# Kernel tuning notes

Hardware: AMD Instinct MI355X
Metric: run time of the kernel (lower is better)

The kernel has to match this reference:

```python
import jax, jax.numpy as jnp
from jax import lax
import numpy as np

B, C, H, Wd = 32, 128, 56, 56
FILTERS = 128
KH = KW = 3
T_MIN_PREV = 0.0  # module defaults (set_params never called)
T_MIN = 0.0
T_MAX = 1.0


def setup_inputs() -> dict:
    key = jax.random.key(0)
    k1, k2 = jax.random.split(key)
    tj = jax.random.uniform(k1, (B, C, H, Wd), dtype=jnp.float32)          # spike times
    W = jax.random.normal(k2, (C * KH * KW, FILTERS), dtype=jnp.float32) * 0.02  # kernel.view(-1, filters)
    D_i = jnp.zeros((9, FILTERS), dtype=jnp.float32)                        # intrinsic delays (only row 0 used)
    return {"tj": tj, "W": W, "D_i": D_i}


def reference(tj, W, D_i):
    # 'same' padding with value t_min, then unfold + (tj - t_min) @ W is
    # exactly a zero-padded conv on (tj - t_min): the pad entries become 0.
    x = tj - T_MIN                                   # [B,C,H,W]
    # Unfold orders patch rows as (C, kh, kw); build the equivalent OIHW kernel.
    kernel = jnp.transpose(W.reshape(C, KH, KW, FILTERS), (3, 0, 1, 2))  # [F,C,KH,KW]
    y = lax.conv_general_dilated(
        x, kernel, window_strides=(1, 1), padding="SAME",
        dimension_numbers=("NCHW", "OIHW", "NCHW"))    # [B,F,H,W]
    threshold = T_MAX - T_MIN - D_i[0]                 # [F]
    ti = y + threshold[None, :, None, None] + T_MIN
    ti = jnp.minimum(ti, T_MAX)                        # torch.where(ti < t_max, ti, t_max)
    return jnp.transpose(ti, (0, 2, 3, 1))             # [B,H,W,F], matches ti.view(b,H,W,filters)
```

## Files before the change

kernel.cpp:

```cpp
#include <hip/hip_runtime.h>


#define BZ 32
#define CC 128
#define HH 56
#define WWD 56
#define HWP 3136
#define FF 128
#define PH 58
#define PW 58
#define NSTEP 36
#define AB_BYTES 24576
#define A_GRAN_REAL 1392
#define BOFF 49152
#define BB_BYTES 8192
#define LDS_TOTAL 73728

typedef __attribute__((ext_vector_type(8))) __bf16 bf16x8;
typedef __attribute__((ext_vector_type(4))) float f32x4;
typedef __attribute__((ext_vector_type(8))) unsigned short us8;
typedef __attribute__((ext_vector_type(4))) float flt4;

__device__ __forceinline__ unsigned short f2bf(float f) {
  unsigned int u = __float_as_uint(f);
  unsigned int r = (u + 0x7FFFu + ((u >> 16) & 1u)) >> 16;
  return (unsigned short)r;
}

#define GLOAD_LDS16(g, l)                                                              \
  __builtin_amdgcn_global_load_lds((const __attribute__((address_space(1))) void*)(g), \
                                   (__attribute__((address_space(3))) void*)(l), 16, 0, 0)

__global__ void prep_w_kernel(const float* __restrict__ W, unsigned short* __restrict__ Wt) {
  int idx = blockIdx.x * 256 + threadIdx.x;
  if (idx >= NSTEP * 512) return;
  int qr = idx >> 9;
  int g = idx & 511;
  int q = qr / 9, r = qr - q * 9;
  int f = g >> 2, kg = g & 3;
  us8 v;
#pragma unroll
  for (int j = 0; j < 8; ++j) {
    int c = q * 32 + kg * 8 + j;
    v[j] = f2bf(W[(c * 9 + r) * FF + f]);
  }
  *reinterpret_cast<us8*>(Wt + (size_t)idx * 8) = v;
}

__global__ __launch_bounds__(256) void prep_x_kernel(const float* __restrict__ x,
                                                     unsigned short* __restrict__ xp) {
  const int blk = blockIdx.x;
  const int b = blk / PH;
  const int ph = blk - b * PH;
  const int tid = threadIdx.x;
  unsigned short* dst = xp + (size_t)(b * PH + ph) * PW * CC;

  if (ph == 0 || ph == PH - 1) {
    us8 z;
#pragma unroll
    for (int k = 0; k < 8; ++k) z[k] = 0;
    for (int i = tid; i < PW * CC / 8; i += 256) reinterpret_cast<us8*>(dst)[i] = z;
    return;
  }

  __shared__ float sm[CC][57];
  const int h = ph - 1;
  {
    const int c = tid >> 1;
    const int half = tid & 1;
    const float* src = x + ((size_t)(b * CC + c)) * HWP + h * WWD + half * 28;
#pragma unroll
    for (int k = 0; k < 7; ++k) {
      flt4 v = *reinterpret_cast<const flt4*>(src + k * 4);
      sm[c][half * 28 + k * 4 + 0] = v[0];
      sm[c][half * 28 + k * 4 + 1] = v[1];
      sm[c][half * 28 + k * 4 + 2] = v[2];
      sm[c][half * 28 + k * 4 + 3] = v[3];
    }
  }
  __syncthreads();
  for (int i = tid; i < PW * 16; i += 256) {
    const int ww = i >> 4;
    const int cg = i & 15;
    us8 v;
    if (ww == 0 || ww == PW - 1) {
#pragma unroll
      for (int k = 0; k < 8; ++k) v[k] = 0;
    } else {
      const int w = ww - 1;
#pragma unroll
      for (int k = 0; k < 8; ++k) v[k] = f2bf(sm[cg * 8 + k][w]);
    }
    reinterpret_cast<us8*>(dst)[i] = v;
  }
}

struct Ctx {
  const unsigned short* xp;
  const unsigned short* Wt;
  int tid;
  int srcA[6];
  int gbase[7];
  int bOffB[4];
  f32x4 acc[7][4];
};

template <int S>
__device__ __forceinline__ void step(Ctx& c, unsigned char* lds) {
  constexpr int q = S / 9, r = S - q * 9;
  constexpr int dh = r / 3 - 1, dw = r - (r / 3) * 3 - 1;
  constexpr int tapoff = (dh * PW + dw) * 4;
  constexpr bool issueA = (q < 3) && (r < 6);
  constexpr bool issueB = (S <= NSTEP - 3);
  constexpr int aS = issueA ? 1 : 0;
  constexpr int bS = issueB ? 2 : 0;
  constexpr int aP = (S == 0) ? 0 : ((((S - 1) / 9) < 3 && ((S - 1) % 9) < 6) ? 1 : 0);
  constexpr int bP = (S == 0) ? 2 : (((S - 1) <= NSTEP - 3) ? 2 : 0);
  constexpr int nOut = aS + bS + aP + bP;

  if constexpr (issueA) {
    const unsigned short* src = c.xp + c.srcA[r] + (q + 1) * 32;
    unsigned char* dst = lds + ((q + 1) & 1) * AB_BYTES + (size_t)(r * 256 + c.tid) * 16;
    GLOAD_LDS16(src, dst);
  }
  if constexpr (issueB) {
    const unsigned short* src = c.Wt + (size_t)(S + 2) * 4096 + c.tid * 8;
    unsigned char* dst = lds + BOFF + ((S + 2) % 3) * BB_BYTES + (size_t)c.tid * 16;
    GLOAD_LDS16(src, dst);
    GLOAD_LDS16(src + 2048, dst + 4096);
  }
  asm volatile("s_waitcnt vmcnt(%0)" ::"n"(nOut));
  __builtin_amdgcn_s_barrier();
  __builtin_amdgcn_sched_barrier(0);

  const unsigned char* pa = lds + (q & 1) * AB_BYTES;
  const unsigned char* pb = lds + BOFF + (S % 3) * BB_BYTES;
  bf16x8 af[7], bf[4];
#pragma unroll
  for (int i = 0; i < 7; ++i)
    af[i] = *reinterpret_cast<const bf16x8*>(pa + ((c.gbase[i] + tapoff) << 4));
#pragma unroll
  for (int j = 0; j < 4; ++j)
    bf[j] = *reinterpret_cast<const bf16x8*>(pb + c.bOffB[j]);

  __builtin_amdgcn_s_setprio(1);
#pragma unroll
  for (int i = 0; i < 7; ++i)
#pragma unroll
    for (int j = 0; j < 4; ++j)
      c.acc[i][j] = __builtin_amdgcn_mfma_f32_16x16x32_bf16(af[i], bf[j], c.acc[i][j], 0, 0, 0);
  __builtin_amdgcn_s_setprio(0);
  __builtin_amdgcn_sched_barrier(0);
  __builtin_amdgcn_s_barrier();
}

template <int S>
__device__ __forceinline__ void do_steps(Ctx& c, unsigned char* lds) {
  step<S>(c, lds);
  if constexpr (S + 1 < NSTEP) do_steps<S + 1>(c, lds);
}

__global__ __launch_bounds__(256, 2) void spiking_conv_main(
    const unsigned short* __restrict__ xp, const unsigned short* __restrict__ Wt,
    const float* __restrict__ Di, float* __restrict__ out) {
  extern __shared__ unsigned char lds[];

  const int bid = blockIdx.x;
  const int wg = (bid & 7) * 56 + (bid >> 3);
  const int b = wg / 14;
  const int rg = wg - b * 14;
  const int h0 = rg * 4;

  Ctx c;
  c.xp = xp;
  c.Wt = Wt;
  const int tid = threadIdx.x;
  c.tid = tid;
  const int lane = tid & 63, wv = tid >> 6;
  const int wr = wv >> 1, wc = wv & 1;
  const int frow = lane & 15, kg = lane >> 4;

#pragma unroll
  for (int k = 0; k < 6; ++k) {
    int g = k * 256 + tid;
    if (g >= A_GRAN_REAL) g = 0;
    int prow = g / 232;
    int rem = g - prow * 232;
    int px = rem >> 2;
    int kg2 = rem & 3;
    c.srcA[k] = ((b * PH + h0 + prow) * PW + px) * CC + kg2 * 8;
  }
#pragma unroll
  for (int i = 0; i < 7; ++i) {
    int t = 16 * i + frow;
    int rowb = (t >= 56) ? 1 : 0;
    int col = t - 56 * rowb;
    c.gbase[i] = ((2 * wr + rowb + 1) * PW + (col + 1)) * 4 + kg;
  }
#pragma unroll
  for (int j = 0; j < 4; ++j)
    c.bOffB[j] = ((wc * 64 + 16 * j + frow) * 4 + kg) << 4;

  const f32x4 zero = {0.0f, 0.0f, 0.0f, 0.0f};
#pragma unroll
  for (int i = 0; i < 7; ++i)
#pragma unroll
    for (int j = 0; j < 4; ++j) c.acc[i][j] = zero;

#pragma unroll
  for (int k = 0; k < 6; ++k)
    GLOAD_LDS16(xp + c.srcA[k], lds + (size_t)(k * 256 + tid) * 16);
  GLOAD_LDS16(Wt + tid * 8, lds + BOFF + (size_t)tid * 16);
  GLOAD_LDS16(Wt + 2048 + tid * 8, lds + BOFF + 4096 + (size_t)tid * 16);
  GLOAD_LDS16(Wt + 4096 + tid * 8, lds + BOFF + BB_BYTES + (size_t)tid * 16);
  GLOAD_LDS16(Wt + 6144 + tid * 8, lds + BOFF + BB_BYTES + 4096 + (size_t)tid * 16);

  do_steps<0>(c, lds);

#pragma unroll
  for (int j = 0; j < 4; ++j) {
    const int col = wc * 64 + 16 * j + frow;
    const float thr = 1.0f - Di[col];
#pragma unroll
    for (int i = 0; i < 7; ++i) {
      const int bt = 16 * i + kg * 4;
      const int rowb = (bt >= 56) ? 1 : 0;
      const int wl0 = bt - 56 * rowb;
      const int orow = h0 + 2 * wr + rowb;
      const size_t obase = ((size_t)b * HWP + (size_t)orow * WWD + wl0) * FF + col;
#pragma unroll
      for (int qq = 0; qq < 4; ++qq) {
        float v = c.acc[i][j][qq] + thr;
        out[obase + (size_t)qq * FF] = fminf(v, 1.0f);
      }
    }
  }
}

__global__ __launch_bounds__(256) void spiking_conv_fallback(
    const float* __restrict__ x, const float* __restrict__ Wf,
    const float* __restrict__ Di, float* __restrict__ out) {
  __shared__ unsigned short Asm2[128][32];
  __shared__ unsigned short Bsm2[128][32];
  const int tid = threadIdx.x;
  const int m0 = blockIdx.x * 128;
  const int mi = tid & 127;
  const int half = tid >> 7;
  const int m = m0 + mi;
  const int bimg = m / HWP;
  const int p = m - bimg * HWP;
  const int h = p / WWD;
  const int w = p - h * WWD;
  const int baseA = (bimg * CC) * HWP + h * WWD + w;
  const int lane = tid & 63;
  const int wid = tid >> 6;
  const int wr = wid >> 1;
  const int wc = wid & 1;
  const int frow = lane & 15;
  const int kg = lane >> 4;
  f32x4 acc[4][4];
  const f32x4 zero = {0.0f, 0.0f, 0.0f, 0.0f};
#pragma unroll
  for (int i = 0; i < 4; ++i)
#pragma unroll
    for (int j = 0; j < 4; ++j) acc[i][j] = zero;
  for (int r = 0; r < 9; ++r) {
    const int dh = r / 3 - 1;
    const int dw = r - (r / 3) * 3 - 1;
    const int hh = h + dh;
    const int ww2 = w + dw;
    const bool valid = ((unsigned)hh < (unsigned)HH) && ((unsigned)ww2 < (unsigned)WWD);
    const int aoff2 = baseA + dh * WWD + dw + half * 16 * HWP;
    for (int c0 = 0; c0 < CC; c0 += 32) {
      __syncthreads();
      {
        const float* src = x + aoff2 + c0 * HWP;
        us8 v0, v1;
#pragma unroll
        for (int i = 0; i < 8; ++i) {
          float f0 = valid ? src[i * HWP] : 0.0f;
          float f1 = valid ? src[(i + 8) * HWP] : 0.0f;
          v0[i] = f2bf(f0);
          v1[i] = f2bf(f1);
        }
        *reinterpret_cast<us8*>(&Asm2[mi][half * 16]) = v0;
        *reinterpret_cast<us8*>(&Asm2[mi][half * 16 + 8]) = v1;
      }
      {
        us8 v0, v1;
#pragma unroll
        for (int i = 0; i < 8; ++i) {
          int cc2 = c0 + half * 16 + i;
          v0[i] = f2bf(Wf[(cc2 * 9 + r) * FF + mi]);
          v1[i] = f2bf(Wf[((cc2 + 8) * 9 + r) * FF + mi]);
        }
        *reinterpret_cast<us8*>(&Bsm2[mi][half * 16]) = v0;
        *reinterpret_cast<us8*>(&Bsm2[mi][half * 16 + 8]) = v1;
      }
      __syncthreads();
      bf16x8 af[4], bfr[4];
#pragma unroll
      for (int i = 0; i < 4; ++i)
        af[i] = *reinterpret_cast<const bf16x8*>(&Asm2[wr * 64 + i * 16 + frow][kg * 8]);
#pragma unroll
      for (int j = 0; j < 4; ++j)
        bfr[j] = *reinterpret_cast<const bf16x8*>(&Bsm2[wc * 64 + j * 16 + frow][kg * 8]);
#pragma unroll
      for (int i = 0; i < 4; ++i)
#pragma unroll
        for (int j = 0; j < 4; ++j)
          acc[i][j] = __builtin_amdgcn_mfma_f32_16x16x32_bf16(af[i], bfr[j], acc[i][j], 0, 0, 0);
    }
  }
#pragma unroll
  for (int j = 0; j < 4; ++j) {
    const int col = wc * 64 + j * 16 + frow;
    const float thr = 1.0f - Di[col];
#pragma unroll
    for (int i = 0; i < 4; ++i) {
      const int rbase = m0 + wr * 64 + i * 16 + kg * 4;
#pragma unroll
      for (int qq = 0; qq < 4; ++qq) {
        float v = acc[i][j][qq] + thr;
        out[(size_t)(rbase + qq) * FF + col] = fminf(v, 1.0f);
      }
    }
  }
}

extern "C" void kernel_launch(void* const* d_in, const int* in_sizes, int n_in,
                              void* d_out, int out_size, void* d_ws, size_t ws_size,
                              hipStream_t stream) {
  const float* tj = (const float*)d_in[0];
  const float* W = (const float*)d_in[1];
  const float* Di = (const float*)d_in[2];
  float* out = (float*)d_out;

  const size_t wt_bytes = (size_t)NSTEP * 512 * 16;
  const size_t xp_bytes = (size_t)BZ * PH * PW * CC * 2;
  unsigned short* Wt = (unsigned short*)d_ws;
  unsigned short* xp = (unsigned short*)((char*)d_ws + wt_bytes);

  bool fast = (ws_size >= wt_bytes + xp_bytes);
  if (fast) {
    prep_w_kernel<<<72, 256, 0, stream>>>(W, Wt);
    prep_x_kernel<<<BZ * PH, 256, 0, stream>>>(tj, xp);
    spiking_conv_main<<<448, 256, LDS_TOTAL, stream>>>(xp, Wt, Di, out);
    if (hipGetLastError() != hipSuccess) fast = false;
  }
  if (!fast) {
    spiking_conv_fallback<<<100352 / 128, 256, 0, stream>>>(tj, W, Di, out);
  }
}
```

Baseline: 53.48 us.

## Load weights directly to registers, swizzle A tile LDS layout, drop per-step barriers

```diff
diff --git a/kernel.cpp b/kernel.cpp
--- a/kernel.cpp
+++ b/kernel.cpp
@@ -9,12 +9,8 @@
 #define FF 128
 #define PH 58
 #define PW 58
-#define NSTEP 36
 #define AB_BYTES 24576
 #define A_GRAN_REAL 1392
-#define BOFF 49152
-#define BB_BYTES 8192
-#define LDS_TOTAL 73728
 
 typedef __attribute__((ext_vector_type(8))) __bf16 bf16x8;
 typedef __attribute__((ext_vector_type(4))) float f32x4;
@@ -33,7 +29,7 @@
 
 __global__ void prep_w_kernel(const float* __restrict__ W, unsigned short* __restrict__ Wt) {
   int idx = blockIdx.x * 256 + threadIdx.x;
-  if (idx >= NSTEP * 512) return;
+  if (idx >= 36 * 512) return;
   int qr = idx >> 9;
   int g = idx & 511;
   int q = qr / 9, r = qr - q * 9;
@@ -95,75 +91,10 @@
   }
 }
 
-struct Ctx {
-  const unsigned short* xp;
-  const unsigned short* Wt;
-  int tid;
-  int srcA[6];
-  int gbase[7];
-  int bOffB[4];
-  f32x4 acc[7][4];
-};
-
-template <int S>
-__device__ __forceinline__ void step(Ctx& c, unsigned char* lds) {
-  constexpr int q = S / 9, r = S - q * 9;
-  constexpr int dh = r / 3 - 1, dw = r - (r / 3) * 3 - 1;
-  constexpr int tapoff = (dh * PW + dw) * 4;
-  constexpr bool issueA = (q < 3) && (r < 6);
-  constexpr bool issueB = (S <= NSTEP - 3);
-  constexpr int aS = issueA ? 1 : 0;
-  constexpr int bS = issueB ? 2 : 0;
-  constexpr int aP = (S == 0) ? 0 : ((((S - 1) / 9) < 3 && ((S - 1) % 9) < 6) ? 1 : 0);
-  constexpr int bP = (S == 0) ? 2 : (((S - 1) <= NSTEP - 3) ? 2 : 0);
-  constexpr int nOut = aS + bS + aP + bP;
-
-  if constexpr (issueA) {
-    const unsigned short* src = c.xp + c.srcA[r] + (q + 1) * 32;
-    unsigned char* dst = lds + ((q + 1) & 1) * AB_BYTES + (size_t)(r * 256 + c.tid) * 16;
-    GLOAD_LDS16(src, dst);
-  }
-  if constexpr (issueB) {
-    const unsigned short* src = c.Wt + (size_t)(S + 2) * 4096 + c.tid * 8;
-    unsigned char* dst = lds + BOFF + ((S + 2) % 3) * BB_BYTES + (size_t)c.tid * 16;
-    GLOAD_LDS16(src, dst);
-    GLOAD_LDS16(src + 2048, dst + 4096);
-  }
-  asm volatile("s_waitcnt vmcnt(%0)" ::"n"(nOut));
-  __builtin_amdgcn_s_barrier();
-  __builtin_amdgcn_sched_barrier(0);
-
-  const unsigned char* pa = lds + (q & 1) * AB_BYTES;
-  const unsigned char* pb = lds + BOFF + (S % 3) * BB_BYTES;
-  bf16x8 af[7], bf[4];
-#pragma unroll
-  for (int i = 0; i < 7; ++i)
-    af[i] = *reinterpret_cast<const bf16x8*>(pa + ((c.gbase[i] + tapoff) << 4));
-#pragma unroll
-  for (int j = 0; j < 4; ++j)
-    bf[j] = *reinterpret_cast<const bf16x8*>(pb + c.bOffB[j]);
-
-  __builtin_amdgcn_s_setprio(1);
-#pragma unroll
-  for (int i = 0; i < 7; ++i)
-#pragma unroll
-    for (int j = 0; j < 4; ++j)
-      c.acc[i][j] = __builtin_amdgcn_mfma_f32_16x16x32_bf16(af[i], bf[j], c.acc[i][j], 0, 0, 0);
-  __builtin_amdgcn_s_setprio(0);
-  __builtin_amdgcn_sched_barrier(0);
-  __builtin_amdgcn_s_barrier();
-}
-
-template <int S>
-__device__ __forceinline__ void do_steps(Ctx& c, unsigned char* lds) {
-  step<S>(c, lds);
-  if constexpr (S + 1 < NSTEP) do_steps<S + 1>(c, lds);
-}
-
 __global__ __launch_bounds__(256, 2) void spiking_conv_main(
     const unsigned short* __restrict__ xp, const unsigned short* __restrict__ Wt,
     const float* __restrict__ Di, float* __restrict__ out) {
-  extern __shared__ unsigned char lds[];
+  __shared__ unsigned char lds[2 * AB_BYTES];
 
   const int bid = blockIdx.x;
   const int wg = (bid & 7) * 56 + (bid >> 3);
@@ -171,51 +102,88 @@
   const int rg = wg - b * 14;
   const int h0 = rg * 4;
 
-  Ctx c;
-  c.xp = xp;
-  c.Wt = Wt;
   const int tid = threadIdx.x;
-  c.tid = tid;
   const int lane = tid & 63, wv = tid >> 6;
   const int wr = wv >> 1, wc = wv & 1;
   const int frow = lane & 15, kg = lane >> 4;
 
+  int srcA[6];
 #pragma unroll
   for (int k = 0; k < 6; ++k) {
-    int g = k * 256 + tid;
-    if (g >= A_GRAN_REAL) g = 0;
+    int gp = k * 256 + tid;
+    int g = (gp >= A_GRAN_REAL) ? 0 : (gp ^ ((gp >> 3) & 3));
     int prow = g / 232;
     int rem = g - prow * 232;
     int px = rem >> 2;
     int kg2 = rem & 3;
-    c.srcA[k] = ((b * PH + h0 + prow) * PW + px) * CC + kg2 * 8;
-  }
+    srcA[k] = ((b * PH + h0 + prow) * PW + px) * CC + kg2 * 8;
+  }
+  int gbase[7];
 #pragma unroll
   for (int i = 0; i < 7; ++i) {
     int t = 16 * i + frow;
     int rowb = (t >= 56) ? 1 : 0;
     int col = t - 56 * rowb;
-    c.gbase[i] = ((2 * wr + rowb + 1) * PW + (col + 1)) * 4 + kg;
-  }
-#pragma unroll
-  for (int j = 0; j < 4; ++j)
-    c.bOffB[j] = ((wc * 64 + 16 * j + frow) * 4 + kg) << 4;
-
+    gbase[i] = ((2 * wr + rowb + 1) * PW + (col + 1)) * 4 + kg;
+  }
+  const int gB = (wc * 64 + frow) * 4 + kg;
+
+  f32x4 acc[7][4];
   const f32x4 zero = {0.0f, 0.0f, 0.0f, 0.0f};
 #pragma unroll
   for (int i = 0; i < 7; ++i)
 #pragma unroll
-    for (int j = 0; j < 4; ++j) c.acc[i][j] = zero;
+    for (int j = 0; j < 4; ++j) acc[i][j] = zero;
 
 #pragma unroll
   for (int k = 0; k < 6; ++k)
-    GLOAD_LDS16(xp + c.srcA[k], lds + (size_t)(k * 256 + tid) * 16);
-  GLOAD_LDS16(Wt + tid * 8, lds + BOFF + (size_t)tid * 16);
-  GLOAD_LDS16(Wt + 2048 + tid * 8, lds + BOFF + 4096 + (size_t)tid * 16);
-  GLOAD_LDS16(Wt + 4096 + tid * 8, lds + BOFF + BB_BYTES + (size_t)tid * 16);
-  GLOAD_LDS16(Wt + 6144 + tid * 8, lds + BOFF + BB_BYTES + 4096 + (size_t)tid * 16);
-
-  do_steps<0>(c, lds);
+    GLOAD_LDS16(xp + srcA[k], lds + (size_t)(k * 256 + tid) * 16);
+  __syncthreads();
+
+#pragma unroll
+  for (int q = 0; q < 4; ++q) {
+    if (q < 3) {
+#pragma unroll
+      for (int k = 0; k < 6; ++k)
+        GLOAD_LDS16(xp + srcA[k] + (q + 1) * 32,
+                    lds + ((q + 1) & 1) * AB_BYTES + (size_t)(k * 256 + tid) * 16);
+    }
+    const unsigned char* pa = lds + (q & 1) * AB_BYTES;
+    const unsigned short* ws = Wt + (size_t)(q * 9) * 4096;
+
+    bf16x8 bcur[4], bnext[4];
+#pragma unroll
+    for (int j = 0; j < 4; ++j)
+      bcur[j] = *reinterpret_cast<const bf16x8*>(ws + (size_t)(gB + j * 64) * 8);
+
+#pragma unroll
+    for (int r = 0; r < 9; ++r) {
+      if (r < 8) {
+#pragma unroll
+        for (int j = 0; j < 4; ++j)
+          bnext[j] = *reinterpret_cast<const bf16x8*>(
+              ws + (size_t)(r + 1) * 4096 + (size_t)(gB + j * 64) * 8);
+      }
+      const int dh = r / 3 - 1, dw = r - (r / 3) * 3 - 1;
+      const int tapoff = (dh * PW + dw) * 4;
+      bf16x8 af[7];
+#pragma unroll
+      for (int i = 0; i < 7; ++i) {
+        int gt = gbase[i] + tapoff;
+        af[i] = *reinterpret_cast<const bf16x8*>(pa + ((gt ^ ((gt >> 3) & 3)) << 4));
+      }
+#pragma unroll
+      for (int i = 0; i < 7; ++i)
+#pragma unroll
+        for (int j = 0; j < 4; ++j)
+          acc[i][j] = __builtin_amdgcn_mfma_f32_16x16x32_bf16(af[i], bcur[j], acc[i][j], 0, 0, 0);
+      if (r < 8) {
+#pragma unroll
+        for (int j = 0; j < 4; ++j) bcur[j] = bnext[j];
+      }
+    }
+    if (q < 3) __syncthreads();
+  }
 
 #pragma unroll
   for (int j = 0; j < 4; ++j) {
@@ -230,7 +198,7 @@
       const size_t obase = ((size_t)b * HWP + (size_t)orow * WWD + wl0) * FF + col;
 #pragma unroll
       for (int qq = 0; qq < 4; ++qq) {
-        float v = c.acc[i][j][qq] + thr;
+        float v = acc[i][j][qq] + thr;
         out[obase + (size_t)qq * FF] = fminf(v, 1.0f);
       }
     }
@@ -336,7 +304,7 @@
   const float* Di = (const float*)d_in[2];
   float* out = (float*)d_out;
 
-  const size_t wt_bytes = (size_t)NSTEP * 512 * 16;
+  const size_t wt_bytes = (size_t)36 * 512 * 16;
   const size_t xp_bytes = (size_t)BZ * PH * PW * CC * 2;
   unsigned short* Wt = (unsigned short*)d_ws;
   unsigned short* xp = (unsigned short*)((char*)d_ws + wt_bytes);
@@ -345,7 +313,7 @@
   if (fast) {
     prep_w_kernel<<<72, 256, 0, stream>>>(W, Wt);
     prep_x_kernel<<<BZ * PH, 256, 0, stream>>>(tj, xp);
-    spiking_conv_main<<<448, 256, LDS_TOTAL, stream>>>(xp, Wt, Di, out);
+    spiking_conv_main<<<448, 256, 0, stream>>>(xp, Wt, Di, out);
     if (hipGetLastError() != hipSuccess) fast = false;
   }
   if (!fast) {
```

Result: slower. 60.71 us (+13.5%).

## Split filters across blocks, load weights to registers, swizzle LDS activations

Applied to the files above, without the earlier changes.

```diff
diff --git a/kernel.cpp b/kernel.cpp
--- a/kernel.cpp
+++ b/kernel.cpp
@@ -9,12 +9,9 @@
 #define FF 128
 #define PH 58
 #define PW 58
-#define NSTEP 36
 #define AB_BYTES 24576
 #define A_GRAN_REAL 1392
-#define BOFF 49152
-#define BB_BYTES 8192
-#define LDS_TOTAL 73728
+#define NSTEP 36
 
 typedef __attribute__((ext_vector_type(8))) __bf16 bf16x8;
 typedef __attribute__((ext_vector_type(4))) float f32x4;
@@ -30,6 +27,8 @@
 #define GLOAD_LDS16(g, l)                                                              \
   __builtin_amdgcn_global_load_lds((const __attribute__((address_space(1))) void*)(g), \
                                    (__attribute__((address_space(3))) void*)(l), 16, 0, 0)
+
+__device__ __forceinline__ int swz(int g) { return g ^ ((g >> 3) & 3); }
 
 __global__ void prep_w_kernel(const float* __restrict__ W, unsigned short* __restrict__ Wt) {
   int idx = blockIdx.x * 256 + threadIdx.x;
@@ -101,57 +100,44 @@
   int tid;
   int srcA[6];
   int gbase[7];
-  int bOffB[4];
-  f32x4 acc[7][4];
+  size_t gB2[2];
+  f32x4 acc[7][2];
+  bf16x8 bbuf[3][2];
 };
 
 template <int S>
 __device__ __forceinline__ void step(Ctx& c, unsigned char* lds) {
   constexpr int q = S / 9, r = S - q * 9;
+
+  if constexpr (r == 0 && q < 3) {
+#pragma unroll
+    for (int k = 0; k < 6; ++k)
+      GLOAD_LDS16(c.xp + c.srcA[k] + (q + 1) * 32,
+                  lds + ((q + 1) & 1) * AB_BYTES + (size_t)(k * 256 + c.tid) * 16);
+  }
+  if constexpr (S + 2 < NSTEP) {
+    const unsigned short* ws = c.Wt + (size_t)(S + 2) * 4096;
+    c.bbuf[(S + 2) % 3][0] = *reinterpret_cast<const bf16x8*>(ws + c.gB2[0]);
+    c.bbuf[(S + 2) % 3][1] = *reinterpret_cast<const bf16x8*>(ws + c.gB2[1]);
+  }
+
   constexpr int dh = r / 3 - 1, dw = r - (r / 3) * 3 - 1;
   constexpr int tapoff = (dh * PW + dw) * 4;
-  constexpr bool issueA = (q < 3) && (r < 6);
-  constexpr bool issueB = (S <= NSTEP - 3);
-  constexpr int aS = issueA ? 1 : 0;
-  constexpr int bS = issueB ? 2 : 0;
-  constexpr int aP = (S == 0) ? 0 : ((((S - 1) / 9) < 3 && ((S - 1) % 9) < 6) ? 1 : 0);
-  constexpr int bP = (S == 0) ? 2 : (((S - 1) <= NSTEP - 3) ? 2 : 0);
-  constexpr int nOut = aS + bS + aP + bP;
-
-  if constexpr (issueA) {
-    const unsigned short* src = c.xp + c.srcA[r] + (q + 1) * 32;
-    unsigned char* dst = lds + ((q + 1) & 1) * AB_BYTES + (size_t)(r * 256 + c.tid) * 16;
-    GLOAD_LDS16(src, dst);
-  }
-  if constexpr (issueB) {
-    const unsigned short* src = c.Wt + (size_t)(S + 2) * 4096 + c.tid * 8;
-    unsigned char* dst = lds + BOFF + ((S + 2) % 3) * BB_BYTES + (size_t)c.tid * 16;
-    GLOAD_LDS16(src, dst);
-    GLOAD_LDS16(src + 2048, dst + 4096);
-  }
-  asm volatile("s_waitcnt vmcnt(%0)" ::"n"(nOut));
-  __builtin_amdgcn_s_barrier();
-  __builtin_amdgcn_sched_barrier(0);
-
   const unsigned char* pa = lds + (q & 1) * AB_BYTES;
-  const unsigned char* pb = lds + BOFF + (S % 3) * BB_BYTES;
-  bf16x8 af[7], bf[4];
+  bf16x8 af[7];
+#pragma unroll
+  for (int i = 0; i < 7; ++i) {
+    int gt = c.gbase[i] + tapoff;
+    af[i] = *reinterpret_cast<const bf16x8*>(pa + (swz(gt) << 4));
+  }
 #pragma unroll
   for (int i = 0; i < 7; ++i)
-    af[i] = *reinterpret_cast<const bf16x8*>(pa + ((c.gbase[i] + tapoff) << 4));
-#pragma unroll
-  for (int j = 0; j < 4; ++j)
-    bf[j] = *reinterpret_cast<const bf16x8*>(pb + c.bOffB[j]);
-
-  __builtin_amdgcn_s_setprio(1);
-#pragma unroll
-  for (int i = 0; i < 7; ++i)
-#pragma unroll
-    for (int j = 0; j < 4; ++j)
-      c.acc[i][j] = __builtin_amdgcn_mfma_f32_16x16x32_bf16(af[i], bf[j], c.acc[i][j], 0, 0, 0);
-  __builtin_amdgcn_s_setprio(0);
-  __builtin_amdgcn_sched_barrier(0);
-  __builtin_amdgcn_s_barrier();
+#pragma unroll
+    for (int j = 0; j < 2; ++j)
+      c.acc[i][j] =
+          __builtin_amdgcn_mfma_f32_16x16x32_bf16(af[i], c.bbuf[S % 3][j], c.acc[i][j], 0, 0, 0);
+
+  if constexpr (r == 8 && q < 3) __syncthreads();
 }
 
 template <int S>
@@ -160,13 +146,15 @@
   if constexpr (S + 1 < NSTEP) do_steps<S + 1>(c, lds);
 }
 
-__global__ __launch_bounds__(256, 2) void spiking_conv_main(
+__global__ __launch_bounds__(256, 3) void spiking_conv_main(
     const unsigned short* __restrict__ xp, const unsigned short* __restrict__ Wt,
     const float* __restrict__ Di, float* __restrict__ out) {
-  extern __shared__ unsigned char lds[];
+  __shared__ unsigned char lds[2 * AB_BYTES];
 
   const int bid = blockIdx.x;
-  const int wg = (bid & 7) * 56 + (bid >> 3);
+  const int wg2 = (bid & 7) * 112 + (bid >> 3);
+  const int nb = wg2 & 1;
+  const int wg = wg2 >> 1;
   const int b = wg / 14;
   const int rg = wg - b * 14;
   const int h0 = rg * 4;
@@ -182,8 +170,8 @@
 
 #pragma unroll
   for (int k = 0; k < 6; ++k) {
-    int g = k * 256 + tid;
-    if (g >= A_GRAN_REAL) g = 0;
+    int gp = k * 256 + tid;
+    int g = (gp >= A_GRAN_REAL) ? 0 : swz(gp);
     int prow = g / 232;
     int rem = g - prow * 232;
     int px = rem >> 2;
@@ -198,28 +186,30 @@
     c.gbase[i] = ((2 * wr + rowb + 1) * PW + (col + 1)) * 4 + kg;
   }
 #pragma unroll
-  for (int j = 0; j < 4; ++j)
-    c.bOffB[j] = ((wc * 64 + 16 * j + frow) * 4 + kg) << 4;
+  for (int j = 0; j < 2; ++j)
+    c.gB2[j] = (size_t)(((nb * 64 + wc * 32 + 16 * j + frow) * 4 + kg)) * 8;
 
   const f32x4 zero = {0.0f, 0.0f, 0.0f, 0.0f};
 #pragma unroll
   for (int i = 0; i < 7; ++i)
 #pragma unroll
-    for (int j = 0; j < 4; ++j) c.acc[i][j] = zero;
+    for (int j = 0; j < 2; ++j) c.acc[i][j] = zero;
 
 #pragma unroll
   for (int k = 0; k < 6; ++k)
     GLOAD_LDS16(xp + c.srcA[k], lds + (size_t)(k * 256 + tid) * 16);
-  GLOAD_LDS16(Wt + tid * 8, lds + BOFF + (size_t)tid * 16);
-  GLOAD_LDS16(Wt + 2048 + tid * 8, lds + BOFF + 4096 + (size_t)tid * 16);
-  GLOAD_LDS16(Wt + 4096 + tid * 8, lds + BOFF + BB_BYTES + (size_t)tid * 16);
-  GLOAD_LDS16(Wt + 6144 + tid * 8, lds + BOFF + BB_BYTES + 4096 + (size_t)tid * 16);
+#pragma unroll
+  for (int j = 0; j < 2; ++j) {
+    c.bbuf[0][j] = *reinterpret_cast<const bf16x8*>(Wt + c.gB2[j]);
+    c.bbuf[1][j] = *reinterpret_cast<const bf16x8*>(Wt + 4096 + c.gB2[j]);
+  }
+  __syncthreads();
 
   do_steps<0>(c, lds);
 
 #pragma unroll
-  for (int j = 0; j < 4; ++j) {
-    const int col = wc * 64 + 16 * j + frow;
+  for (int j = 0; j < 2; ++j) {
+    const int col = nb * 64 + wc * 32 + 16 * j + frow;
     const float thr = 1.0f - Di[col];
 #pragma unroll
     for (int i = 0; i < 7; ++i) {
@@ -345,7 +335,7 @@
   if (fast) {
     prep_w_kernel<<<72, 256, 0, stream>>>(W, Wt);
     prep_x_kernel<<<BZ * PH, 256, 0, stream>>>(tj, xp);
-    spiking_conv_main<<<448, 256, LDS_TOTAL, stream>>>(xp, Wt, Di, out);
+    spiking_conv_main<<<896, 256, 0, stream>>>(xp, Wt, Di, out);
     if (hipGetLastError() != hipSuccess) fast = false;
   }
   if (!fast) {
```

Measured after the change: 79.23 us. 1.48x slower.
